# Kernel optimization log

Hardware: AMD Instinct MI355X
Metric: run time of the kernel (lower is better)

Reference implementation:

```python
import jax, jax.numpy as jnp
import numpy as np

S, V, E, H = 4096, 10000, 128, 256
NE, TK, NH, HD, FF, NL = 4, 2, 4, 64, 2048, 2
EPS = 1e-5
SCALE = 1.0 / np.sqrt(HD).astype(np.float32)


def setup_inputs() -> dict:
    key = jax.random.key(0)
    ks = iter(jax.random.split(key, 64))
    n = lambda shape: jax.random.normal(next(ks), shape, jnp.float32) * 0.02
    inp = {"x": jax.random.randint(next(ks), (S,), 0, V)}
    inp["emb"] = n((V, E))
    for i, din in enumerate([E, H, H]):
        inp[f"moe{i}_gw"] = n((NE, din))
        inp[f"moe{i}_gb"] = jnp.zeros((NE,), jnp.float32)
        inp[f"moe{i}_ew"] = n((NE, H, din))
        inp[f"moe{i}_eb"] = jnp.zeros((NE, H), jnp.float32)
    inp["attn_in_w"] = n((NL, 3 * H, H)); inp["attn_in_b"] = jnp.zeros((NL, 3 * H), jnp.float32)
    inp["attn_out_w"] = n((NL, H, H));    inp["attn_out_b"] = jnp.zeros((NL, H), jnp.float32)
    inp["ln1_g"] = jnp.ones((NL, H), jnp.float32); inp["ln1_b"] = jnp.zeros((NL, H), jnp.float32)
    inp["ln2_g"] = jnp.ones((NL, H), jnp.float32); inp["ln2_b"] = jnp.zeros((NL, H), jnp.float32)
    inp["ff1_w"] = n((NL, FF, H)); inp["ff1_b"] = jnp.zeros((NL, FF), jnp.float32)
    inp["ff2_w"] = n((NL, H, FF)); inp["ff2_b"] = jnp.zeros((NL, H), jnp.float32)
    inp["fc_w"] = n((H, H)); inp["fc_b"] = jnp.zeros((H,), jnp.float32)
    inp["out_w"] = n((V, H)); inp["out_b"] = jnp.zeros((V,), jnp.float32)
    return inp


def _ln(x, g, b):
    m = x.mean(-1, keepdims=True)
    v = ((x - m) ** 2).mean(-1, keepdims=True)
    return (x - m) * jax.lax.rsqrt(v + EPS) * g + b


def _moe(x, gw, gb, ew, eb):
    # x: [S, din]. Faithful quirk: experts are the top-k of TOKEN 0's gates,
    # applied to every token, weighted by each token's own top-k gate scores.
    scores = jax.nn.softmax(x @ gw.T + gb, axis=-1)            # [S, NE]
    vals, idx = jax.lax.top_k(scores, TK)                      # [S, TK]
    sel = idx[0]                                               # [TK]
    outs = jnp.einsum('si,khi->skh', x, ew[sel]) + eb[sel][None]  # [S, TK, H]
    return (outs * vals[:, :, None]).sum(axis=1)               # [S, H]


def reference(x, emb,
              moe0_gw, moe0_gb, moe0_ew, moe0_eb,
              moe1_gw, moe1_gb, moe1_ew, moe1_eb,
              moe2_gw, moe2_gb, moe2_ew, moe2_eb,
              attn_in_w, attn_in_b, attn_out_w, attn_out_b,
              ln1_g, ln1_b, ln2_g, ln2_b,
              ff1_w, ff1_b, ff2_w, ff2_b,
              fc_w, fc_b, out_w, out_b):
    h = emb[x]                                                 # [S, E]
    for gw, gb, ew, eb in [(moe0_gw, moe0_gb, moe0_ew, moe0_eb),
                           (moe1_gw, moe1_gb, moe1_ew, moe1_eb),
                           (moe2_gw, moe2_gb, moe2_ew, moe2_eb)]:
        h = _moe(h, gw, gb, ew, eb)                            # [S, H]
    for l in range(NL):  # post-norm TransformerEncoderLayer (relu, no dropout at eval)
        qkv = h @ attn_in_w[l].T + attn_in_b[l]                # [S, 3H]
        q, k, v = [t.reshape(S, NH, HD) for t in jnp.split(qkv, 3, axis=-1)]
        att = jax.nn.softmax(jnp.einsum('shd,thd->hst', q, k) * SCALE, axis=-1)
        a = jnp.einsum('hst,thd->shd', att, v).reshape(S, H)
        h = _ln(h + a @ attn_out_w[l].T + attn_out_b[l], ln1_g[l], ln1_b[l])
        ffh = jax.nn.relu(h @ ff1_w[l].T + ff1_b[l]) @ ff2_w[l].T + ff2_b[l]
        h = _ln(h + ffh, ln2_g[l], ln2_b[l])
    h = h @ fc_w.T + fc_b                                      # [S, H]
    logits = h @ out_w.T + out_b                               # [S, V]
    return jax.nn.log_softmax(logits, axis=-1)
```

## Files before the change

### kernel.cpp

```cpp
#include <hip/hip_runtime.h>
#include <math.h>

#define S_ 4096
#define V_ 10000
#define E_ 128
#define H_ 256
#define NE_ 4
#define NH_ 4
#define HD_ 64
#define FF_ 2048
#define NL_ 2
#define EPS_ 1e-5f
#define SCALE_ 0.125f
#define SPLITS_ 4
#define PSTRIDE_ 160

typedef __attribute__((ext_vector_type(8))) short bf16x8;
typedef __attribute__((ext_vector_type(4))) float f32x4;

static __device__ __forceinline__ short f2bf(float f) {
  unsigned u = __builtin_bit_cast(unsigned, f);
  unsigned r = (u + 0x7fffu + ((u >> 16) & 1u)) >> 16;
  return (short)r;
}
static __device__ __forceinline__ float bf2f(short s) {
  unsigned u = ((unsigned)(unsigned short)s) << 16;
  return __builtin_bit_cast(float, u);
}

struct CvtArgs {
  const float* src[9];
  short* dst[9];
  int pfx[10];
};
__global__ __launch_bounds__(256) void k_cvt(CvtArgs a) {
  int b = blockIdx.x, s = 0;
  while (b >= a.pfx[s + 1]) ++s;
  size_t base = (size_t)(b - a.pfx[s]) * 2048 + threadIdx.x * 8;
  const float* sp = a.src[s] + base;
  short* dp = a.dst[s] + base;
  float4 v0 = *(const float4*)sp;
  float4 v1 = *(const float4*)(sp + 4);
  short4 o0, o1;
  o0.x = f2bf(v0.x); o0.y = f2bf(v0.y); o0.z = f2bf(v0.z); o0.w = f2bf(v0.w);
  o1.x = f2bf(v1.x); o1.y = f2bf(v1.y); o1.z = f2bf(v1.z); o1.w = f2bf(v1.w);
  *(short4*)dp = o0;
  *(short4*)(dp + 4) = o1;
}

__global__ __launch_bounds__(256) void k_embed(const int* __restrict__ x,
                                               const float* __restrict__ emb,
                                               short* __restrict__ h) {
  int i4 = (blockIdx.x * 256 + threadIdx.x) * 4;
  int s = i4 >> 7, e = i4 & 127;
  float4 v = *(const float4*)&emb[(size_t)x[s] * E_ + e];
  short4 o;
  o.x = f2bf(v.x); o.y = f2bf(v.y); o.z = f2bf(v.z); o.w = f2bf(v.w);
  *(short4*)&h[i4] = o;
}

__global__ __launch_bounds__(256) void k_gates(const short* __restrict__ X, int din,
                                               const float* __restrict__ gw,
                                               const float* __restrict__ gb,
                                               float* __restrict__ vals,
                                               int* __restrict__ sel) {
  int wave = threadIdx.x >> 6, lane = threadIdx.x & 63;
  int s = blockIdx.x * 4 + wave;
  const short* xs = X + (size_t)s * din;
  float a0 = 0.f, a1 = 0.f, a2 = 0.f, a3 = 0.f;
  for (int i = lane; i < din; i += 64) {
    float xv = bf2f(xs[i]);
    a0 += xv * gw[0 * din + i];
    a1 += xv * gw[1 * din + i];
    a2 += xv * gw[2 * din + i];
    a3 += xv * gw[3 * din + i];
  }
#pragma unroll
  for (int off = 32; off > 0; off >>= 1) {
    a0 += __shfl_xor(a0, off, 64);
    a1 += __shfl_xor(a1, off, 64);
    a2 += __shfl_xor(a2, off, 64);
    a3 += __shfl_xor(a3, off, 64);
  }
  if (lane == 0) {
    float sc[4] = {a0 + gb[0], a1 + gb[1], a2 + gb[2], a3 + gb[3]};
    float mx = fmaxf(fmaxf(sc[0], sc[1]), fmaxf(sc[2], sc[3]));
    float sum = 0.f;
#pragma unroll
    for (int e = 0; e < 4; ++e) { sc[e] = expf(sc[e] - mx); sum += sc[e]; }
    float inv = 1.0f / sum;
#pragma unroll
    for (int e = 0; e < 4; ++e) sc[e] *= inv;
    int i0 = 0; float v0 = sc[0];
#pragma unroll
    for (int e = 1; e < 4; ++e) if (sc[e] > v0) { v0 = sc[e]; i0 = e; }
    float v1 = -1.0f; int i1 = 0;
#pragma unroll
    for (int e = 0; e < 4; ++e) if (e != i0 && sc[e] > v1) { v1 = sc[e]; i1 = e; }
    vals[2 * s + 0] = v0;
    vals[2 * s + 1] = v1;
    if (s == 0) { sel[0] = i0; sel[1] = i1; }
  }
}

template <int ACT>
__global__ __launch_bounds__(256) void k_gemm64(const short* __restrict__ A,
                                                const short* __restrict__ W,
                                                const float* __restrict__ bias,
                                                short* __restrict__ C,
                                                int M, int N, int K) {
  __shared__ short As[64][40];
  __shared__ short Bs[64][40];
  int bm = blockIdx.y * 64, bn = blockIdx.x * 64;
  int tid = threadIdx.x, lane = tid & 63, wv = tid >> 6;
  int quad = lane >> 4, m16 = lane & 15;
  int wr = (wv >> 1) * 32, wc = (wv & 1) * 32;
  int srow = tid >> 2, sc = (tid & 3) * 8;
  const short* Ar = A + (size_t)(bm + srow) * K + sc;
  const short* Wr = W + (size_t)(bn + srow) * K + sc;
  f32x4 acc[2][2];
#pragma unroll
  for (int m = 0; m < 2; ++m)
#pragma unroll
    for (int n = 0; n < 2; ++n) acc[m][n] = (f32x4){0.f, 0.f, 0.f, 0.f};
  for (int k0 = 0; k0 < K; k0 += 32) {
    *(bf16x8*)&As[srow][sc] = *(const bf16x8*)&Ar[k0];
    *(bf16x8*)&Bs[srow][sc] = *(const bf16x8*)&Wr[k0];
    __syncthreads();
    bf16x8 af[2], bf[2];
#pragma unroll
    for (int m = 0; m < 2; ++m) af[m] = *(const bf16x8*)&As[wr + m * 16 + m16][quad * 8];
#pragma unroll
    for (int n = 0; n < 2; ++n) bf[n] = *(const bf16x8*)&Bs[wc + n * 16 + m16][quad * 8];
#pragma unroll
    for (int m = 0; m < 2; ++m)
#pragma unroll
      for (int n = 0; n < 2; ++n)
        acc[m][n] = __builtin_amdgcn_mfma_f32_16x16x32_bf16(af[m], bf[n], acc[m][n], 0, 0, 0);
    __syncthreads();
  }
#pragma unroll
  for (int n = 0; n < 2; ++n) {
    int col = bn + wc + n * 16 + m16;
    float b = bias[col];
#pragma unroll
    for (int m = 0; m < 2; ++m) {
      int row0 = bm + wr + m * 16 + quad * 4;
#pragma unroll
      for (int r = 0; r < 4; ++r) {
        float v = acc[m][n][r] + b;
        if (ACT) v = fmaxf(v, 0.f);
        C[(size_t)(row0 + r) * N + col] = f2bf(v);
      }
    }
  }
}

template <int ACT>
__global__ __launch_bounds__(256) void k_gemm32(const short* __restrict__ A,
                                                const short* __restrict__ W,
                                                const float* __restrict__ bias,
                                                short* __restrict__ C,
                                                int M, int N, int K) {
  __shared__ short As[32][40];
  __shared__ short Bs[64][40];
  int bm = blockIdx.y * 32, bn = blockIdx.x * 64;
  int tid = threadIdx.x, lane = tid & 63, wv = tid >> 6;
  int quad = lane >> 4, m16 = lane & 15;
  int wr = (wv >> 1) * 16, wc = (wv & 1) * 32;
  int srow = tid >> 2, sc = (tid & 3) * 8;
  const short* Ar = A + (size_t)(bm + (srow & 31)) * K + sc;
  const short* Wr = W + (size_t)(bn + srow) * K + sc;
  f32x4 acc[2];
  acc[0] = (f32x4){0.f, 0.f, 0.f, 0.f};
  acc[1] = (f32x4){0.f, 0.f, 0.f, 0.f};
  for (int k0 = 0; k0 < K; k0 += 32) {
    if (tid < 128) *(bf16x8*)&As[srow][sc] = *(const bf16x8*)&Ar[k0];
    *(bf16x8*)&Bs[srow][sc] = *(const bf16x8*)&Wr[k0];
    __syncthreads();
    bf16x8 af = *(const bf16x8*)&As[wr + m16][quad * 8];
    bf16x8 bf0 = *(const bf16x8*)&Bs[wc + m16][quad * 8];
    bf16x8 bf1 = *(const bf16x8*)&Bs[wc + 16 + m16][quad * 8];
    acc[0] = __builtin_amdgcn_mfma_f32_16x16x32_bf16(af, bf0, acc[0], 0, 0, 0);
    acc[1] = __builtin_amdgcn_mfma_f32_16x16x32_bf16(af, bf1, acc[1], 0, 0, 0);
    __syncthreads();
  }
#pragma unroll
  for (int n = 0; n < 2; ++n) {
    int col = bn + wc + n * 16 + m16;
    float b = bias[col];
    int row0 = bm + wr + quad * 4;
#pragma unroll
    for (int r = 0; r < 4; ++r) {
      float v = acc[n][r] + b;
      if (ACT) v = fmaxf(v, 0.f);
      C[(size_t)(row0 + r) * N + col] = f2bf(v);
    }
  }
}

__global__ __launch_bounds__(256) void k_moe(const short* __restrict__ A,
                                             const short* __restrict__ EW,
                                             const float* __restrict__ EB,
                                             const float* __restrict__ vals,
                                             const int* __restrict__ sel,
                                             short* __restrict__ C,
                                             int N, int K) {
  __shared__ short As[32][40];
  __shared__ short B0s[64][40];
  __shared__ short B1s[64][40];
  int e0 = sel[0], e1 = sel[1];
  const short* W0 = EW + (size_t)e0 * N * K;
  const short* W1 = EW + (size_t)e1 * N * K;
  const float* b0 = EB + (size_t)e0 * N;
  const float* b1 = EB + (size_t)e1 * N;
  int bm = blockIdx.y * 32, bn = blockIdx.x * 64;
  int tid = threadIdx.x, lane = tid & 63, wv = tid >> 6;
  int quad = lane >> 4, m16 = lane & 15;
  int wr = (wv >> 1) * 16, wc = (wv & 1) * 32;
  int srow = tid >> 2, sc = (tid & 3) * 8;
  const short* Ar = A + (size_t)(bm + (srow & 31)) * K + sc;
  const short* W0r = W0 + (size_t)(bn + srow) * K + sc;
  const short* W1r = W1 + (size_t)(bn + srow) * K + sc;
  f32x4 a0[2], a1[2];
  a0[0] = a0[1] = (f32x4){0.f, 0.f, 0.f, 0.f};
  a1[0] = a1[1] = (f32x4){0.f, 0.f, 0.f, 0.f};
  for (int k0 = 0; k0 < K; k0 += 32) {
    if (tid < 128) *(bf16x8*)&As[srow][sc] = *(const bf16x8*)&Ar[k0];
    *(bf16x8*)&B0s[srow][sc] = *(const bf16x8*)&W0r[k0];
    *(bf16x8*)&B1s[srow][sc] = *(const bf16x8*)&W1r[k0];
    __syncthreads();
    bf16x8 af = *(const bf16x8*)&As[wr + m16][quad * 8];
#pragma unroll
    for (int n = 0; n < 2; ++n) {
      bf16x8 bf0 = *(const bf16x8*)&B0s[wc + n * 16 + m16][quad * 8];
      bf16x8 bf1 = *(const bf16x8*)&B1s[wc + n * 16 + m16][quad * 8];
      a0[n] = __builtin_amdgcn_mfma_f32_16x16x32_bf16(af, bf0, a0[n], 0, 0, 0);
      a1[n] = __builtin_amdgcn_mfma_f32_16x16x32_bf16(af, bf1, a1[n], 0, 0, 0);
    }
    __syncthreads();
  }
#pragma unroll
  for (int n = 0; n < 2; ++n) {
    int col = bn + wc + n * 16 + m16;
    float bb0 = b0[col], bb1 = b1[col];
    int row0 = bm + wr + quad * 4;
#pragma unroll
    for (int r = 0; r < 4; ++r) {
      int row = row0 + r;
      float v = vals[2 * row] * (a0[n][r] + bb0) + vals[2 * row + 1] * (a1[n][r] + bb1);
      C[(size_t)row * N + col] = f2bf(v);
    }
  }
}

template <int ACT>
__global__ __launch_bounds__(256) void k_gemm128(const short* __restrict__ A,
                                                 const short* __restrict__ W,
                                                 const float* __restrict__ bias,
                                                 short* __restrict__ C,
                                                 int M, int N, int K) {
  __shared__ short As[128][40];
  __shared__ short Bs[128][40];
  int bm = blockIdx.y * 128, bn = blockIdx.x * 128;
  int tid = threadIdx.x, lane = tid & 63, wv = tid >> 6;
  int quad = lane >> 4, m16 = lane & 15;
  int wr = (wv >> 1) * 64, wc = (wv & 1) * 64;
  int srow = tid >> 1, sc = (tid & 1) * 16;
  const short* Ar = A + (size_t)(bm + srow) * K + sc;
  const short* Wr = W + (size_t)(bn + srow) * K + sc;
  f32x4 acc[4][4];
#pragma unroll
  for (int m = 0; m < 4; ++m)
#pragma unroll
    for (int n = 0; n < 4; ++n) acc[m][n] = (f32x4){0.f, 0.f, 0.f, 0.f};
  for (int k0 = 0; k0 < K; k0 += 32) {
    *(bf16x8*)&As[srow][sc] = *(const bf16x8*)&Ar[k0];
    *(bf16x8*)&As[srow][sc + 8] = *(const bf16x8*)&Ar[k0 + 8];
    *(bf16x8*)&Bs[srow][sc] = *(const bf16x8*)&Wr[k0];
    *(bf16x8*)&Bs[srow][sc + 8] = *(const bf16x8*)&Wr[k0 + 8];
    __syncthreads();
    bf16x8 af[4], bf[4];
#pragma unroll
    for (int m = 0; m < 4; ++m) af[m] = *(const bf16x8*)&As[wr + m * 16 + m16][quad * 8];
#pragma unroll
    for (int n = 0; n < 4; ++n) bf[n] = *(const bf16x8*)&Bs[wc + n * 16 + m16][quad * 8];
#pragma unroll
    for (int m = 0; m < 4; ++m)
#pragma unroll
      for (int n = 0; n < 4; ++n)
        acc[m][n] = __builtin_amdgcn_mfma_f32_16x16x32_bf16(af[m], bf[n], acc[m][n], 0, 0, 0);
    __syncthreads();
  }
#pragma unroll
  for (int n = 0; n < 4; ++n) {
    int col = bn + wc + n * 16 + m16;
    float b = bias[col];
#pragma unroll
    for (int m = 0; m < 4; ++m) {
      int row0 = bm + wr + m * 16 + quad * 4;
#pragma unroll
      for (int r = 0; r < 4; ++r) {
        float v = acc[m][n][r] + b;
        if (ACT) v = fmaxf(v, 0.f);
        C[(size_t)(row0 + r) * N + col] = f2bf(v);
      }
    }
  }
}

__global__ __launch_bounds__(256) void k_glogits(const short* __restrict__ A,
                                                 const short* __restrict__ W,
                                                 const float* __restrict__ bias,
                                                 float* __restrict__ C,
                                                 float* __restrict__ psums,
                                                 int M, int N, int K) {
  __shared__ short As[128][40];
  __shared__ short Bs[128][40];
  int bm = blockIdx.y * 128, bn = blockIdx.x * 128;
  int tid = threadIdx.x, lane = tid & 63, wv = tid >> 6;
  int quad = lane >> 4, m16 = lane & 15;
  int wr = (wv >> 1) * 64, wc = (wv & 1) * 64;
  int srow = tid >> 1, sc = (tid & 1) * 16;
  const short* Ar = A + (size_t)(bm + srow) * K + sc;
  int br = bn + srow;
  const short* Wr = W + (size_t)(br < N ? br : N - 1) * K + sc;
  f32x4 acc[4][4];
#pragma unroll
  for (int m = 0; m < 4; ++m)
#pragma unroll
    for (int n = 0; n < 4; ++n) acc[m][n] = (f32x4){0.f, 0.f, 0.f, 0.f};
  for (int k0 = 0; k0 < K; k0 += 32) {
    *(bf16x8*)&As[srow][sc] = *(const bf16x8*)&Ar[k0];
    *(bf16x8*)&As[srow][sc + 8] = *(const bf16x8*)&Ar[k0 + 8];
    *(bf16x8*)&Bs[srow][sc] = *(const bf16x8*)&Wr[k0];
    *(bf16x8*)&Bs[srow][sc + 8] = *(const bf16x8*)&Wr[k0 + 8];
    __syncthreads();
    bf16x8 af[4], bf[4];
#pragma unroll
    for (int m = 0; m < 4; ++m) af[m] = *(const bf16x8*)&As[wr + m * 16 + m16][quad * 8];
#pragma unroll
    for (int n = 0; n < 4; ++n) bf[n] = *(const bf16x8*)&Bs[wc + n * 16 + m16][quad * 8];
#pragma unroll
    for (int m = 0; m < 4; ++m)
#pragma unroll
      for (int n = 0; n < 4; ++n)
        acc[m][n] = __builtin_amdgcn_mfma_f32_16x16x32_bf16(af[m], bf[n], acc[m][n], 0, 0, 0);
    __syncthreads();
  }
  float bcol[4];
  int cvalid[4];
#pragma unroll
  for (int n = 0; n < 4; ++n) {
    int col = bn + wc + n * 16 + m16;
    cvalid[n] = (col < N);
    bcol[n] = cvalid[n] ? bias[col] : 0.f;
  }
  int pslot = blockIdx.x * 2 + (wv & 1);
#pragma unroll
  for (int m = 0; m < 4; ++m) {
#pragma unroll
    for (int r = 0; r < 4; ++r) {
      int row = bm + wr + m * 16 + quad * 4 + r;
      float es = 0.f;
#pragma unroll
      for (int n = 0; n < 4; ++n) {
        if (cvalid[n]) {
          float v = acc[m][n][r] + bcol[n];
          C[(size_t)row * N + (bn + wc + n * 16 + m16)] = v;
          es += __expf(v);
        }
      }
#pragma unroll
      for (int mask = 1; mask < 16; mask <<= 1) es += __shfl_xor(es, mask, 16);
      if (m16 == 0) psums[(size_t)row * PSTRIDE_ + pslot] = es;
    }
  }
}

__global__ __launch_bounds__(256) void k_lsfinal(float* __restrict__ out,
                                                 const float* __restrict__ psums,
                                                 int nslots) {
  __shared__ float rbuf[256];
  int s = blockIdx.x, t = threadIdx.x;
  rbuf[t] = (t < nslots) ? psums[(size_t)s * PSTRIDE_ + t] : 0.f;
  __syncthreads();
#pragma unroll
  for (int o = 128; o > 0; o >>= 1) {
    if (t < o) rbuf[t] += rbuf[t + o];
    __syncthreads();
  }
  float lse = logf(rbuf[0]);
  float4* row = (float4*)(out + (size_t)s * V_);
  for (int i = t; i < V_ / 4; i += 256) {
    float4 o4 = row[i];
    o4.x -= lse; o4.y -= lse; o4.z -= lse; o4.w -= lse;
    row[i] = o4;
  }
}

__global__ __launch_bounds__(256) void k_attn(const short* __restrict__ qkv,
                                              float* __restrict__ Opart,
                                              float* __restrict__ Lpart) {
  __shared__ short Ks[64][72];
  __shared__ short Vt[64][72];
  int tid = threadIdx.x, lane = tid & 63, wv = tid >> 6;
  int quad = lane >> 4, m16 = lane & 15;
  int head = blockIdx.y, hd0 = head * HD_;
  int split = blockIdx.z;
  int qbase = blockIdx.x * 64 + wv * 16;
  bf16x8 qf[2];
  {
    const short* qr = qkv + (size_t)(qbase + m16) * (3 * H_) + hd0 + quad * 8;
    qf[0] = *(const bf16x8*)&qr[0];
    qf[1] = *(const bf16x8*)&qr[32];
  }
  f32x4 o[4];
#pragma unroll
  for (int dt = 0; dt < 4; ++dt) o[dt] = (f32x4){0.f, 0.f, 0.f, 0.f};
  float l = 0.f;

  int kb_end = (split + 1) * (S_ / 64 / SPLITS_);
  for (int kb = split * (S_ / 64 / SPLITS_); kb < kb_end; ++kb) {
    __syncthreads();
    {
      int key = tid >> 2, d0 = (tid & 3) * 16;
      const short* kr = qkv + (size_t)(kb * 64 + key) * (3 * H_) + H_ + hd0 + d0;
      *(bf16x8*)&Ks[key][d0] = *(const bf16x8*)&kr[0];
      *(bf16x8*)&Ks[key][d0 + 8] = *(const bf16x8*)&kr[8];
    }
    {
      int key0 = (tid & 15) * 4, d0 = (tid >> 4) * 4;
      const short* vbase = qkv + (size_t)(kb * 64 + key0) * (3 * H_) + 2 * H_ + hd0 + d0;
      short4 v0 = *(const short4*)&vbase[0];
      short4 v1 = *(const short4*)&vbase[3 * H_];
      short4 v2 = *(const short4*)&vbase[6 * H_];
      short4 v3 = *(const short4*)&vbase[9 * H_];
      short4 t0 = {v0.x, v1.x, v2.x, v3.x};
      short4 t1 = {v0.y, v1.y, v2.y, v3.y};
      short4 t2 = {v0.z, v1.z, v2.z, v3.z};
      short4 t3 = {v0.w, v1.w, v2.w, v3.w};
      *(short4*)&Vt[d0 + 0][key0] = t0;
      *(short4*)&Vt[d0 + 1][key0] = t1;
      *(short4*)&Vt[d0 + 2][key0] = t2;
      *(short4*)&Vt[d0 + 3][key0] = t3;
    }
    __syncthreads();
    f32x4 s4[4];
#pragma unroll
    for (int kt = 0; kt < 4; ++kt) {
      bf16x8 ak0 = *(const bf16x8*)&Ks[kt * 16 + m16][quad * 8];
      bf16x8 ak1 = *(const bf16x8*)&Ks[kt * 16 + m16][32 + quad * 8];
      f32x4 z = (f32x4){0.f, 0.f, 0.f, 0.f};
      z = __builtin_amdgcn_mfma_f32_16x16x32_bf16(ak0, qf[0], z, 0, 0, 0);
      z = __builtin_amdgcn_mfma_f32_16x16x32_bf16(ak1, qf[1], z, 0, 0, 0);
      s4[kt] = z;
    }
    float rsum = 0.f;
    unsigned pw[4][2];
#pragma unroll
    for (int kt = 0; kt < 4; ++kt) {
      float p0 = __expf(s4[kt][0] * SCALE_);
      float p1 = __expf(s4[kt][1] * SCALE_);
      float p2 = __expf(s4[kt][2] * SCALE_);
      float p3 = __expf(s4[kt][3] * SCALE_);
      rsum += (p0 + p1) + (p2 + p3);
      asm("v_cvt_pk_bf16_f32 %0, %1, %2" : "=v"(pw[kt][0]) : "v"(p0), "v"(p1));
      asm("v_cvt_pk_bf16_f32 %0, %1, %2" : "=v"(pw[kt][1]) : "v"(p2), "v"(p3));
    }
    {
      unsigned ua = __builtin_bit_cast(unsigned, rsum), ub = ua;
      asm volatile("v_permlane16_swap_b32 %0, %1" : "+v"(ua), "+v"(ub));
      float s01 = __builtin_bit_cast(float, ua) + __builtin_bit_cast(float, ub);
      unsigned uc = __builtin_bit_cast(unsigned, s01), ud = uc;
      asm volatile("v_permlane32_swap_b32 %0, %1" : "+v"(uc), "+v"(ud));
      l += __builtin_bit_cast(float, uc) + __builtin_bit_cast(float, ud);
    }
#pragma unroll
    for (int c = 0; c < 2; ++c) {
      unsigned a0 = pw[2 * c][0], b0 = pw[2 * c + 1][0];
      asm volatile("v_permlane32_swap_b32 %0, %1" : "+v"(a0), "+v"(b0));
      asm volatile("v_permlane16_swap_b32 %0, %1" : "+v"(a0), "+v"(b0));
      unsigned a1 = pw[2 * c][1], b1 = pw[2 * c + 1][1];
      asm volatile("v_permlane32_swap_b32 %0, %1" : "+v"(a1), "+v"(b1));
      asm volatile("v_permlane16_swap_b32 %0, %1" : "+v"(a1), "+v"(b1));
      union { unsigned u[4]; bf16x8 v; } pu;
      pu.u[0] = a0;
      pu.u[1] = a1;
      pu.u[2] = b0;
      pu.u[3] = b1;
      bf16x8 pa = pu.v;
#pragma unroll
      for (int dt = 0; dt < 4; ++dt) {
        bf16x8 bv = *(const bf16x8*)&Vt[dt * 16 + m16][c * 32 + quad * 8];
        o[dt] = __builtin_amdgcn_mfma_f32_16x16x32_bf16(pa, bv, o[dt], 0, 0, 0);
      }
    }
  }
  float* Op = Opart + ((size_t)(split * NH_ + head) * S_) * 64;
#pragma unroll
  for (int dt = 0; dt < 4; ++dt) {
#pragma unroll
    for (int r = 0; r < 4; ++r) {
      int row = qbase + quad * 4 + r;
      Op[(size_t)row * 64 + dt * 16 + m16] = o[dt][r];
    }
  }
  if (quad == 0) {
    float* Lp = Lpart + (size_t)(split * NH_ + head) * S_;
    Lp[qbase + m16] = l;
  }
}

__global__ __launch_bounds__(256) void k_att_combine(const float* __restrict__ Opart,
                                                     const float* __restrict__ Lpart,
                                                     short* __restrict__ abuf) {
  int idx = blockIdx.x * 256 + threadIdx.x;
  int s = idx >> 8, hd = idx & 255;
  int head = hd >> 6, d = hd & 63;
  float num = 0.f, den = 0.f;
#pragma unroll
  for (int sp = 0; sp < SPLITS_; ++sp) {
    num += Opart[((size_t)(sp * NH_ + head) * S_ + s) * 64 + d];
    den += Lpart[(size_t)(sp * NH_ + head) * S_ + s];
  }
  abuf[idx] = f2bf(num / den);
}

__global__ __launch_bounds__(256) void k_add_ln(short* __restrict__ h,
                                                const short* __restrict__ t_,
                                                const float* __restrict__ g,
                                                const float* __restrict__ b) {
  int wv = threadIdx.x >> 6, lane = threadIdx.x & 63;
  int s = blockIdx.x * 4 + wv;
  size_t off = (size_t)s * H_ + lane * 4;
  short4 hv = *(const short4*)&h[off];
  short4 tv = *(const short4*)&t_[off];
  float x[4] = {bf2f(hv.x) + bf2f(tv.x), bf2f(hv.y) + bf2f(tv.y),
                bf2f(hv.z) + bf2f(tv.z), bf2f(hv.w) + bf2f(tv.w)};
  float sum = x[0] + x[1] + x[2] + x[3];
#pragma unroll
  for (int mask = 1; mask < 64; mask <<= 1) sum += __shfl_xor(sum, mask, 64);
  float mean = sum * (1.0f / H_);
  float d[4], vs = 0.f;
#pragma unroll
  for (int i = 0; i < 4; ++i) { d[i] = x[i] - mean; vs += d[i] * d[i]; }
#pragma unroll
  for (int mask = 1; mask < 64; mask <<= 1) vs += __shfl_xor(vs, mask, 64);
  float inv = rsqrtf(vs * (1.0f / H_) + EPS_);
  float4 gv = *(const float4*)&g[lane * 4];
  float4 bv = *(const float4*)&b[lane * 4];
  short4 ov;
  ov.x = f2bf(d[0] * inv * gv.x + bv.x);
  ov.y = f2bf(d[1] * inv * gv.y + bv.y);
  ov.z = f2bf(d[2] * inv * gv.z + bv.z);
  ov.w = f2bf(d[3] * inv * gv.w + bv.w);
  *(short4*)&h[off] = ov;
}

extern "C" void kernel_launch(void* const* d_in, const int* in_sizes, int n_in,
                              void* d_out, int out_size, void* d_ws, size_t ws_size,
                              hipStream_t stream) {
  const int* x = (const int*)d_in[0];
  const float* emb = (const float*)d_in[1];
  const float* moe_gw[3] = {(const float*)d_in[2], (const float*)d_in[6], (const float*)d_in[10]};
  const float* moe_gb[3] = {(const float*)d_in[3], (const float*)d_in[7], (const float*)d_in[11]};
  const float* moe_eb[3] = {(const float*)d_in[5], (const float*)d_in[9], (const float*)d_in[13]};
  const float* attn_in_b = (const float*)d_in[15];
  const float* attn_out_b = (const float*)d_in[17];
  const float* ln1_g = (const float*)d_in[18];
  const float* ln1_b = (const float*)d_in[19];
  const float* ln2_g = (const float*)d_in[20];
  const float* ln2_b = (const float*)d_in[21];
  const float* ff1_b = (const float*)d_in[23];
  const float* ff2_b = (const float*)d_in[25];
  const float* fc_b = (const float*)d_in[27];
  const float* out_b = (const float*)d_in[29];
  float* out = (float*)d_out;

  short* wsS = (short*)d_ws;
  size_t off = 0;
  auto alloc = [&](size_t n) { short* p = wsS + off; off += n; return p; };
  short* ewb0 = alloc(131072);
  short* ewb1 = alloc(262144);
  short* ewb2 = alloc(262144);
  short* aiwb = alloc(393216);
  short* aowb = alloc(131072);
  short* f1wb = alloc(1048576);
  short* f2wb = alloc(1048576);
  short* fcwb = alloc(65536);
  short* owb  = alloc(2560000);
  short* hb_e = alloc((size_t)S_ * E_);
  short* hb_a = alloc((size_t)S_ * H_);
  short* hb_b = alloc((size_t)S_ * H_);
  short* qkvb = alloc((size_t)S_ * 3 * H_);
  short* abufb = alloc((size_t)S_ * H_);
  short* tmpb = alloc((size_t)S_ * H_);
  short* ffhb = alloc((size_t)S_ * FF_);
  float* vals = (float*)(wsS + off); off += 2 * (size_t)S_ * 2;
  int* sel = (int*)(wsS + off);
  float* Opart = (float*)ffhb;
  float* Lpart = (float*)tmpb;
  float* psums = (float*)f1wb;

  const short* moe_ewb[3] = {ewb0, ewb1, ewb2};

  CvtArgs ca;
  ca.src[0] = (const float*)d_in[4];  ca.dst[0] = ewb0;
  ca.src[1] = (const float*)d_in[8];  ca.dst[1] = ewb1;
  ca.src[2] = (const float*)d_in[12]; ca.dst[2] = ewb2;
  ca.src[3] = (const float*)d_in[14]; ca.dst[3] = aiwb;
  ca.src[4] = (const float*)d_in[16]; ca.dst[4] = aowb;
  ca.src[5] = (const float*)d_in[22]; ca.dst[5] = f1wb;
  ca.src[6] = (const float*)d_in[24]; ca.dst[6] = f2wb;
  ca.src[7] = (const float*)d_in[26]; ca.dst[7] = fcwb;
  ca.src[8] = (const float*)d_in[28]; ca.dst[8] = owb;
  int sizes[9] = {131072, 262144, 262144, 393216, 131072, 1048576, 1048576, 65536, 2560000};
  ca.pfx[0] = 0;
  for (int i = 0; i < 9; ++i) ca.pfx[i + 1] = ca.pfx[i] + sizes[i] / 2048;
  k_cvt<<<dim3(ca.pfx[9]), dim3(256), 0, stream>>>(ca);

  k_embed<<<dim3(S_ * E_ / 1024), dim3(256), 0, stream>>>(x, emb, hb_e);

  const short* moe_in[3] = {hb_e, hb_a, hb_b};
  short* moe_out[3] = {hb_a, hb_b, hb_a};
  int moe_k[3] = {E_, H_, H_};
  for (int i = 0; i < 3; ++i) {
    k_gates<<<dim3(S_ / 4), dim3(256), 0, stream>>>(moe_in[i], moe_k[i], moe_gw[i], moe_gb[i], vals, sel);
    k_moe<<<dim3(H_ / 64, S_ / 32), dim3(256), 0, stream>>>(moe_in[i], moe_ewb[i], moe_eb[i],
                                                            vals, sel, moe_out[i], H_, moe_k[i]);
  }

  for (int l = 0; l < NL_; ++l) {
    k_gemm64<0><<<dim3(3 * H_ / 64, S_ / 64), dim3(256), 0, stream>>>(
        hb_a, aiwb + (size_t)l * 3 * H_ * H_, attn_in_b + (size_t)l * 3 * H_, qkvb, S_, 3 * H_, H_);
    k_attn<<<dim3(S_ / 64, NH_, SPLITS_), dim3(256), 0, stream>>>(qkvb, Opart, Lpart);
    k_att_combine<<<dim3(S_ * H_ / 256), dim3(256), 0, stream>>>(Opart, Lpart, abufb);
    k_gemm32<0><<<dim3(H_ / 64, S_ / 32), dim3(256), 0, stream>>>(
        abufb, aowb + (size_t)l * H_ * H_, attn_out_b + (size_t)l * H_, tmpb, S_, H_, H_);
    k_add_ln<<<dim3(S_ / 4), dim3(256), 0, stream>>>(hb_a, tmpb, ln1_g + l * H_, ln1_b + l * H_);
    k_gemm128<1><<<dim3(FF_ / 128, S_ / 128), dim3(256), 0, stream>>>(
        hb_a, f1wb + (size_t)l * FF_ * H_, ff1_b + (size_t)l * FF_, ffhb, S_, FF_, H_);
    k_gemm32<0><<<dim3(H_ / 64, S_ / 32), dim3(256), 0, stream>>>(
        ffhb, f2wb + (size_t)l * H_ * FF_, ff2_b + (size_t)l * H_, tmpb, S_, H_, FF_);
    k_add_ln<<<dim3(S_ / 4), dim3(256), 0, stream>>>(hb_a, tmpb, ln2_g + l * H_, ln2_b + l * H_);
  }

  k_gemm32<0><<<dim3(H_ / 64, S_ / 32), dim3(256), 0, stream>>>(hb_a, fcwb, fc_b, tmpb, S_, H_, H_);
  int nxb = (V_ + 127) / 128;
  k_glogits<<<dim3(nxb, S_ / 128), dim3(256), 0, stream>>>(tmpb, owb, out_b, out, psums, S_, V_, H_);
  k_lsfinal<<<dim3(S_), dim3(256), 0, stream>>>(out, psums, nxb * 2);
}
```

Baseline: 613.7 us.

## Recompute logits GEMM instead of re-reading output; double query tiles in attention

The logits stage is restructured into three passes. The first GEMM computes only the per-row exp partial sums, a small kernel reduces them to a log-sum-exp, and a second GEMM recomputes the logits and writes them already normalised. This removes the read-modify-write pass over the 4096x10000 float output at the cost of running the K=256 GEMM twice. Separately, each attention block now handles 128 queries instead of 64, reusing each loaded K/V tile across twice as many queries, at the price of more registers and half as many blocks.

```diff
diff --git a/kernel.cpp b/kernel.cpp
--- a/kernel.cpp
+++ b/kernel.cpp
@@ -309,12 +309,11 @@
   }
 }
 
-__global__ __launch_bounds__(256) void k_glogits(const short* __restrict__ A,
-                                                 const short* __restrict__ W,
-                                                 const float* __restrict__ bias,
-                                                 float* __restrict__ C,
-                                                 float* __restrict__ psums,
-                                                 int M, int N, int K) {
+__global__ __launch_bounds__(256) void k_gsum(const short* __restrict__ A,
+                                              const short* __restrict__ W,
+                                              const float* __restrict__ bias,
+                                              float* __restrict__ psums,
+                                              int M, int N, int K) {
   __shared__ short As[128][40];
   __shared__ short Bs[128][40];
   int bm = blockIdx.y * 128, bn = blockIdx.x * 128;
@@ -367,7 +366,6 @@
       for (int n = 0; n < 4; ++n) {
         if (cvalid[n]) {
           float v = acc[m][n][r] + bcol[n];
-          C[(size_t)row * N + (bn + wc + n * 16 + m16)] = v;
           es += __expf(v);
         }
       }
@@ -378,24 +376,78 @@
   }
 }
 
-__global__ __launch_bounds__(256) void k_lsfinal(float* __restrict__ out,
-                                                 const float* __restrict__ psums,
-                                                 int nslots) {
-  __shared__ float rbuf[256];
-  int s = blockIdx.x, t = threadIdx.x;
-  rbuf[t] = (t < nslots) ? psums[(size_t)s * PSTRIDE_ + t] : 0.f;
-  __syncthreads();
-#pragma unroll
-  for (int o = 128; o > 0; o >>= 1) {
-    if (t < o) rbuf[t] += rbuf[t + o];
-    __syncthreads();
-  }
-  float lse = logf(rbuf[0]);
-  float4* row = (float4*)(out + (size_t)s * V_);
-  for (int i = t; i < V_ / 4; i += 256) {
-    float4 o4 = row[i];
-    o4.x -= lse; o4.y -= lse; o4.z -= lse; o4.w -= lse;
-    row[i] = o4;
+__global__ __launch_bounds__(256) void k_lse(const float* __restrict__ psums,
+                                             float* __restrict__ lse, int nslots) {
+  int wv = threadIdx.x >> 6, lane = threadIdx.x & 63;
+  int s = blockIdx.x * 4 + wv;
+  float a = 0.f;
+  for (int i = lane; i < nslots; i += 64) a += psums[(size_t)s * PSTRIDE_ + i];
+#pragma unroll
+  for (int mask = 1; mask < 64; mask <<= 1) a += __shfl_xor(a, mask, 64);
+  if (lane == 0) lse[s] = logf(a);
+}
+
+__global__ __launch_bounds__(256) void k_gout(const short* __restrict__ A,
+                                              const short* __restrict__ W,
+                                              const float* __restrict__ bias,
+                                              const float* __restrict__ lse,
+                                              float* __restrict__ C,
+                                              int M, int N, int K) {
+  __shared__ short As[128][40];
+  __shared__ short Bs[128][40];
+  int bm = blockIdx.y * 128, bn = blockIdx.x * 128;
+  int tid = threadIdx.x, lane = tid & 63, wv = tid >> 6;
+  int quad = lane >> 4, m16 = lane & 15;
+  int wr = (wv >> 1) * 64, wc = (wv & 1) * 64;
+  int srow = tid >> 1, sc = (tid & 1) * 16;
+  const short* Ar = A + (size_t)(bm + srow) * K + sc;
+  int br = bn + srow;
+  const short* Wr = W + (size_t)(br < N ? br : N - 1) * K + sc;
+  f32x4 acc[4][4];
+#pragma unroll
+  for (int m = 0; m < 4; ++m)
+#pragma unroll
+    for (int n = 0; n < 4; ++n) acc[m][n] = (f32x4){0.f, 0.f, 0.f, 0.f};
+  for (int k0 = 0; k0 < K; k0 += 32) {
+    *(bf16x8*)&As[srow][sc] = *(const bf16x8*)&Ar[k0];
+    *(bf16x8*)&As[srow][sc + 8] = *(const bf16x8*)&Ar[k0 + 8];
+    *(bf16x8*)&Bs[srow][sc] = *(const bf16x8*)&Wr[k0];
+    *(bf16x8*)&Bs[srow][sc + 8] = *(const bf16x8*)&Wr[k0 + 8];
+    __syncthreads();
+    bf16x8 af[4], bf[4];
+#pragma unroll
+    for (int m = 0; m < 4; ++m) af[m] = *(const bf16x8*)&As[wr + m * 16 + m16][quad * 8];
+#pragma unroll
+    for (int n = 0; n < 4; ++n) bf[n] = *(const bf16x8*)&Bs[wc + n * 16 + m16][quad * 8];
+#pragma unroll
+    for (int m = 0; m < 4; ++m)
+#pragma unroll
+      for (int n = 0; n < 4; ++n)
+        acc[m][n] = __builtin_amdgcn_mfma_f32_16x16x32_bf16(af[m], bf[n], acc[m][n], 0, 0, 0);
+    __syncthreads();
+  }
+  float bcol[4];
+  int cvalid[4];
+#pragma unroll
+  for (int n = 0; n < 4; ++n) {
+    int col = bn + wc + n * 16 + m16;
+    cvalid[n] = (col < N);
+    bcol[n] = cvalid[n] ? bias[col] : 0.f;
+  }
+#pragma unroll
+  for (int m = 0; m < 4; ++m) {
+#pragma unroll
+    for (int r = 0; r < 4; ++r) {
+      int row = bm + wr + m * 16 + quad * 4 + r;
+      float flse = lse[row];
+#pragma unroll
+      for (int n = 0; n < 4; ++n) {
+        if (cvalid[n]) {
+          float v = acc[m][n][r] + bcol[n] - flse;
+          C[(size_t)row * N + (bn + wc + n * 16 + m16)] = v;
+        }
+      }
+    }
   }
 }
 
@@ -408,17 +460,24 @@
   int quad = lane >> 4, m16 = lane & 15;
   int head = blockIdx.y, hd0 = head * HD_;
   int split = blockIdx.z;
-  int qbase = blockIdx.x * 64 + wv * 16;
-  bf16x8 qf[2];
+  int qbaseA = blockIdx.x * 128 + wv * 16;
+  int qbaseB = qbaseA + 64;
+  bf16x8 qfA[2], qfB[2];
   {
-    const short* qr = qkv + (size_t)(qbase + m16) * (3 * H_) + hd0 + quad * 8;
-    qf[0] = *(const bf16x8*)&qr[0];
-    qf[1] = *(const bf16x8*)&qr[32];
-  }
-  f32x4 o[4];
-#pragma unroll
-  for (int dt = 0; dt < 4; ++dt) o[dt] = (f32x4){0.f, 0.f, 0.f, 0.f};
-  float l = 0.f;
+    const short* qrA = qkv + (size_t)(qbaseA + m16) * (3 * H_) + hd0 + quad * 8;
+    qfA[0] = *(const bf16x8*)&qrA[0];
+    qfA[1] = *(const bf16x8*)&qrA[32];
+    const short* qrB = qkv + (size_t)(qbaseB + m16) * (3 * H_) + hd0 + quad * 8;
+    qfB[0] = *(const bf16x8*)&qrB[0];
+    qfB[1] = *(const bf16x8*)&qrB[32];
+  }
+  f32x4 oA[4], oB[4];
+#pragma unroll
+  for (int dt = 0; dt < 4; ++dt) {
+    oA[dt] = (f32x4){0.f, 0.f, 0.f, 0.f};
+    oB[dt] = (f32x4){0.f, 0.f, 0.f, 0.f};
+  }
+  float lA = 0.f, lB = 0.f;
 
   int kb_end = (split + 1) * (S_ / 64 / SPLITS_);
   for (int kb = split * (S_ / 64 / SPLITS_); kb < kb_end; ++kb) {
@@ -446,54 +505,84 @@
       *(short4*)&Vt[d0 + 3][key0] = t3;
     }
     __syncthreads();
-    f32x4 s4[4];
+    f32x4 sA[4], sB[4];
 #pragma unroll
     for (int kt = 0; kt < 4; ++kt) {
       bf16x8 ak0 = *(const bf16x8*)&Ks[kt * 16 + m16][quad * 8];
       bf16x8 ak1 = *(const bf16x8*)&Ks[kt * 16 + m16][32 + quad * 8];
-      f32x4 z = (f32x4){0.f, 0.f, 0.f, 0.f};
-      z = __builtin_amdgcn_mfma_f32_16x16x32_bf16(ak0, qf[0], z, 0, 0, 0);
-      z = __builtin_amdgcn_mfma_f32_16x16x32_bf16(ak1, qf[1], z, 0, 0, 0);
-      s4[kt] = z;
-    }
-    float rsum = 0.f;
-    unsigned pw[4][2];
-#pragma unroll
-    for (int kt = 0; kt < 4; ++kt) {
-      float p0 = __expf(s4[kt][0] * SCALE_);
-      float p1 = __expf(s4[kt][1] * SCALE_);
-      float p2 = __expf(s4[kt][2] * SCALE_);
-      float p3 = __expf(s4[kt][3] * SCALE_);
-      rsum += (p0 + p1) + (p2 + p3);
-      asm("v_cvt_pk_bf16_f32 %0, %1, %2" : "=v"(pw[kt][0]) : "v"(p0), "v"(p1));
-      asm("v_cvt_pk_bf16_f32 %0, %1, %2" : "=v"(pw[kt][1]) : "v"(p2), "v"(p3));
-    }
+      f32x4 zA = (f32x4){0.f, 0.f, 0.f, 0.f};
+      zA = __builtin_amdgcn_mfma_f32_16x16x32_bf16(ak0, qfA[0], zA, 0, 0, 0);
+      zA = __builtin_amdgcn_mfma_f32_16x16x32_bf16(ak1, qfA[1], zA, 0, 0, 0);
+      sA[kt] = zA;
+      f32x4 zB = (f32x4){0.f, 0.f, 0.f, 0.f};
+      zB = __builtin_amdgcn_mfma_f32_16x16x32_bf16(ak0, qfB[0], zB, 0, 0, 0);
+      zB = __builtin_amdgcn_mfma_f32_16x16x32_bf16(ak1, qfB[1], zB, 0, 0, 0);
+      sB[kt] = zB;
+    }
+    unsigned pwA[4][2], pwB[4][2];
     {
+      float rsum = 0.f;
+#pragma unroll
+      for (int kt = 0; kt < 4; ++kt) {
+        float p0 = __expf(sA[kt][0] * SCALE_);
+        float p1 = __expf(sA[kt][1] * SCALE_);
+        float p2 = __expf(sA[kt][2] * SCALE_);
+        float p3 = __expf(sA[kt][3] * SCALE_);
+        rsum += (p0 + p1) + (p2 + p3);
+        asm("v_cvt_pk_bf16_f32 %0, %1, %2" : "=v"(pwA[kt][0]) : "v"(p0), "v"(p1));
+        asm("v_cvt_pk_bf16_f32 %0, %1, %2" : "=v"(pwA[kt][1]) : "v"(p2), "v"(p3));
+      }
       unsigned ua = __builtin_bit_cast(unsigned, rsum), ub = ua;
       asm volatile("v_permlane16_swap_b32 %0, %1" : "+v"(ua), "+v"(ub));
       float s01 = __builtin_bit_cast(float, ua) + __builtin_bit_cast(float, ub);
       unsigned uc = __builtin_bit_cast(unsigned, s01), ud = uc;
       asm volatile("v_permlane32_swap_b32 %0, %1" : "+v"(uc), "+v"(ud));
-      l += __builtin_bit_cast(float, uc) + __builtin_bit_cast(float, ud);
+      lA += __builtin_bit_cast(float, uc) + __builtin_bit_cast(float, ud);
+    }
+    {
+      float rsum = 0.f;
+#pragma unroll
+      for (int kt = 0; kt < 4; ++kt) {
+        float p0 = __expf(sB[kt][0] * SCALE_);
+        float p1 = __expf(sB[kt][1] * SCALE_);
+        float p2 = __expf(sB[kt][2] * SCALE_);
+        float p3 = __expf(sB[kt][3] * SCALE_);
+        rsum += (p0 + p1) + (p2 + p3);
+        asm("v_cvt_pk_bf16_f32 %0, %1, %2" : "=v"(pwB[kt][0]) : "v"(p0), "v"(p1));
+        asm("v_cvt_pk_bf16_f32 %0, %1, %2" : "=v"(pwB[kt][1]) : "v"(p2), "v"(p3));
+      }
+      unsigned ua = __builtin_bit_cast(unsigned, rsum), ub = ua;
+      asm volatile("v_permlane16_swap_b32 %0, %1" : "+v"(ua), "+v"(ub));
+      float s01 = __builtin_bit_cast(float, ua) + __builtin_bit_cast(float, ub);
+      unsigned uc = __builtin_bit_cast(unsigned, s01), ud = uc;
+      asm volatile("v_permlane32_swap_b32 %0, %1" : "+v"(uc), "+v"(ud));
+      lB += __builtin_bit_cast(float, uc) + __builtin_bit_cast(float, ud);
     }
 #pragma unroll
     for (int c = 0; c < 2; ++c) {
-      unsigned a0 = pw[2 * c][0], b0 = pw[2 * c + 1][0];
+      unsigned a0 = pwA[2 * c][0], b0 = pwA[2 * c + 1][0];
       asm volatile("v_permlane32_swap_b32 %0, %1" : "+v"(a0), "+v"(b0));
       asm volatile("v_permlane16_swap_b32 %0, %1" : "+v"(a0), "+v"(b0));
-      unsigned a1 = pw[2 * c][1], b1 = pw[2 * c + 1][1];
+      unsigned a1 = pwA[2 * c][1], b1 = pwA[2 * c + 1][1];
       asm volatile("v_permlane32_swap_b32 %0, %1" : "+v"(a1), "+v"(b1));
       asm volatile("v_permlane16_swap_b32 %0, %1" : "+v"(a1), "+v"(b1));
-      union { unsigned u[4]; bf16x8 v; } pu;
-      pu.u[0] = a0;
-      pu.u[1] = a1;
-      pu.u[2] = b0;
-      pu.u[3] = b1;
-      bf16x8 pa = pu.v;
+      union { unsigned u[4]; bf16x8 v; } puA;
+      puA.u[0] = a0; puA.u[1] = a1; puA.u[2] = b0; puA.u[3] = b1;
+      bf16x8 paA = puA.v;
+      unsigned c0 = pwB[2 * c][0], d0w = pwB[2 * c + 1][0];
+      asm volatile("v_permlane32_swap_b32 %0, %1" : "+v"(c0), "+v"(d0w));
+      asm volatile("v_permlane16_swap_b32 %0, %1" : "+v"(c0), "+v"(d0w));
+      unsigned c1 = pwB[2 * c][1], d1w = pwB[2 * c + 1][1];
+      asm volatile("v_permlane32_swap_b32 %0, %1" : "+v"(c1), "+v"(d1w));
+      asm volatile("v_permlane16_swap_b32 %0, %1" : "+v"(c1), "+v"(d1w));
+      union { unsigned u[4]; bf16x8 v; } puB;
+      puB.u[0] = c0; puB.u[1] = c1; puB.u[2] = d0w; puB.u[3] = d1w;
+      bf16x8 paB = puB.v;
 #pragma unroll
       for (int dt = 0; dt < 4; ++dt) {
         bf16x8 bv = *(const bf16x8*)&Vt[dt * 16 + m16][c * 32 + quad * 8];
-        o[dt] = __builtin_amdgcn_mfma_f32_16x16x32_bf16(pa, bv, o[dt], 0, 0, 0);
+        oA[dt] = __builtin_amdgcn_mfma_f32_16x16x32_bf16(paA, bv, oA[dt], 0, 0, 0);
+        oB[dt] = __builtin_amdgcn_mfma_f32_16x16x32_bf16(paB, bv, oB[dt], 0, 0, 0);
       }
     }
   }
@@ -502,13 +591,16 @@
   for (int dt = 0; dt < 4; ++dt) {
 #pragma unroll
     for (int r = 0; r < 4; ++r) {
-      int row = qbase + quad * 4 + r;
-      Op[(size_t)row * 64 + dt * 16 + m16] = o[dt][r];
+      int rowA = qbaseA + quad * 4 + r;
+      Op[(size_t)rowA * 64 + dt * 16 + m16] = oA[dt][r];
+      int rowB = qbaseB + quad * 4 + r;
+      Op[(size_t)rowB * 64 + dt * 16 + m16] = oB[dt][r];
     }
   }
   if (quad == 0) {
     float* Lp = Lpart + (size_t)(split * NH_ + head) * S_;
-    Lp[qbase + m16] = l;
+    Lp[qbaseA + m16] = lA;
+    Lp[qbaseB + m16] = lB;
   }
 }
 
@@ -602,6 +694,7 @@
   float* Opart = (float*)ffhb;
   float* Lpart = (float*)tmpb;
   float* psums = (float*)f1wb;
+  float* lse = psums + (size_t)S_ * PSTRIDE_;
 
   const short* moe_ewb[3] = {ewb0, ewb1, ewb2};
 
@@ -634,7 +727,7 @@
   for (int l = 0; l < NL_; ++l) {
     k_gemm64<0><<<dim3(3 * H_ / 64, S_ / 64), dim3(256), 0, stream>>>(
         hb_a, aiwb + (size_t)l * 3 * H_ * H_, attn_in_b + (size_t)l * 3 * H_, qkvb, S_, 3 * H_, H_);
-    k_attn<<<dim3(S_ / 64, NH_, SPLITS_), dim3(256), 0, stream>>>(qkvb, Opart, Lpart);
+    k_attn<<<dim3(S_ / 128, NH_, SPLITS_), dim3(256), 0, stream>>>(qkvb, Opart, Lpart);
     k_att_combine<<<dim3(S_ * H_ / 256), dim3(256), 0, stream>>>(Opart, Lpart, abufb);
     k_gemm32<0><<<dim3(H_ / 64, S_ / 32), dim3(256), 0, stream>>>(
         abufb, aowb + (size_t)l * H_ * H_, attn_out_b + (size_t)l * H_, tmpb, S_, H_, H_);
@@ -648,6 +741,7 @@
 
   k_gemm32<0><<<dim3(H_ / 64, S_ / 32), dim3(256), 0, stream>>>(hb_a, fcwb, fc_b, tmpb, S_, H_, H_);
   int nxb = (V_ + 127) / 128;
-  k_glogits<<<dim3(nxb, S_ / 128), dim3(256), 0, stream>>>(tmpb, owb, out_b, out, psums, S_, V_, H_);
-  k_lsfinal<<<dim3(S_), dim3(256), 0, stream>>>(out, psums, nxb * 2);
-}
+  k_gsum<<<dim3(nxb, S_ / 128), dim3(256), 0, stream>>>(tmpb, owb, out_b, psums, S_, V_, H_);
+  k_lse<<<dim3(S_ / 4), dim3(256), 0, stream>>>(psums, lse, nxb * 2);
+  k_gout<<<dim3(nxb, S_ / 128), dim3(256), 0, stream>>>(tmpb, owb, out_b, lse, out, S_, V_, H_);
+}
```

Result: faster. 597.7 us (-2.6%).
